# Kernel optimization log

Hardware: AMD Instinct MI355X
Metric: run time of the kernel (lower is better)

## Reference

```python
import jax, jax.numpy as jnp
import numpy as np

N_NODES = 50000
N_EDGES = 800000
DIMS = [100, 512, 256, 128, 200]  # input -> conv1 -> conv2 -> conv3 -> conv4


def setup_inputs() -> dict:
    key = jax.random.key(0)
    ks = jax.random.split(key, 2 + 4)
    x = jax.random.normal(ks[0], (N_NODES, DIMS[0]), dtype=jnp.float32)
    edge_index = jax.random.randint(ks[1], (2, N_EDGES), 0, N_NODES, dtype=jnp.int64)
    inp = {"x": x, "edge_index": edge_index}
    for i in range(4):
        fan_in = DIMS[i]
        W = jax.random.normal(ks[2 + i], (DIMS[i], DIMS[i + 1]), dtype=jnp.float32) * (1.0 / np.sqrt(fan_in)).astype(np.float32)
        b = jnp.zeros((DIMS[i + 1],), dtype=jnp.float32)
        inp[f"W{i + 1}"] = W
        inp[f"b{i + 1}"] = b
    return inp


def _gcn_layer(x, row, col, norm, W, b, n):
    # PyG GCNConv: linear transform first, then normalized scatter-add, then bias.
    h = x @ W                           # [N, out]
    msg = h[row] * norm[:, None]        # [E+N, out] gather + edge scale
    agg = jax.ops.segment_sum(msg, col, num_segments=n)  # scatter-add to targets
    return agg + b


def reference(x, edge_index, W1, b1, W2, b2, W3, b3, W4, b4):
    n = x.shape[0]
    loop = jnp.arange(n, dtype=edge_index.dtype)
    row = jnp.concatenate([edge_index[0], loop])  # sources (with self-loops)
    col = jnp.concatenate([edge_index[1], loop])  # targets (with self-loops)
    deg = jax.ops.segment_sum(jnp.ones_like(col, dtype=x.dtype), col, num_segments=n)
    dinv = jnp.where(deg > 0, jax.lax.rsqrt(deg), 0.0)
    norm = dinv[row] * dinv[col]  # symmetric D^{-1/2}(A+I)D^{-1/2} edge weights

    out = jax.nn.relu(_gcn_layer(x, row, col, norm, W1, b1, n))
    out = jax.nn.relu(_gcn_layer(out, row, col, norm, W2, b2, n))
    out = jax.nn.relu(_gcn_layer(out, row, col, norm, W3, b3, n))
    out = jax.nn.relu(_gcn_layer(out, row, col, norm, W4, b4, n))
    return jnp.mean(out, axis=0, keepdims=True)  # [1, 200]
```

## Files before the change

### kernel.cpp

```cpp
#include <hip/hip_runtime.h>
#include <hip/hip_bf16.h>


#define NN 50000
#define NE 800000
#define PRANGE (NN / 8)
#define CAP 96

typedef __attribute__((ext_vector_type(8))) _Float16 f16x8;
typedef __attribute__((ext_vector_type(4))) float floatx4;
typedef __attribute__((ext_vector_type(2))) float floatx2;

union U16x8 {
    uint4 u4;
    f16x8 h;
    _Float16 e[8];
};

__device__ __forceinline__ void dec16(const unsigned char* p, float* f) {
    uint4 v = *(const uint4*)p;
    unsigned w[4] = {v.x, v.y, v.z, v.w};
#pragma unroll
    for (int k = 0; k < 4; k++) {
        floatx2 lo = __builtin_amdgcn_cvt_pk_f32_fp8(w[k], false);
        floatx2 hi = __builtin_amdgcn_cvt_pk_f32_fp8(w[k], true);
        f[k * 4 + 0] = lo[0];
        f[k * 4 + 1] = lo[1];
        f[k * 4 + 2] = hi[0];
        f[k * 4 + 3] = hi[1];
    }
}

__device__ __forceinline__ uint4 enc16(const float* f) {
    uint4 r;
    unsigned w;
    w = __builtin_amdgcn_cvt_pk_fp8_f32(f[0], f[1], 0, false);
    w = __builtin_amdgcn_cvt_pk_fp8_f32(f[2], f[3], (int)w, true);
    r.x = w;
    w = __builtin_amdgcn_cvt_pk_fp8_f32(f[4], f[5], 0, false);
    w = __builtin_amdgcn_cvt_pk_fp8_f32(f[6], f[7], (int)w, true);
    r.y = w;
    w = __builtin_amdgcn_cvt_pk_fp8_f32(f[8], f[9], 0, false);
    w = __builtin_amdgcn_cvt_pk_fp8_f32(f[10], f[11], (int)w, true);
    r.z = w;
    w = __builtin_amdgcn_cvt_pk_fp8_f32(f[12], f[13], 0, false);
    w = __builtin_amdgcn_cvt_pk_fp8_f32(f[14], f[15], (int)w, true);
    r.w = w;
    return r;
}

__device__ __forceinline__ uint4 dec8_f16(uint2 v) {
    floatx2 f0 = __builtin_amdgcn_cvt_pk_f32_fp8(v.x, false);
    floatx2 f1 = __builtin_amdgcn_cvt_pk_f32_fp8(v.x, true);
    floatx2 f2 = __builtin_amdgcn_cvt_pk_f32_fp8(v.y, false);
    floatx2 f3 = __builtin_amdgcn_cvt_pk_f32_fp8(v.y, true);
    U16x8 o;
    o.e[0] = (_Float16)f0[0]; o.e[1] = (_Float16)f0[1];
    o.e[2] = (_Float16)f1[0]; o.e[3] = (_Float16)f1[1];
    o.e[4] = (_Float16)f2[0]; o.e[5] = (_Float16)f2[1];
    o.e[6] = (_Float16)f3[0]; o.e[7] = (_Float16)f3[1];
    return o.u4;
}

__global__ __launch_bounds__(256) void setup_kernel(
    const void* __restrict__ ei, unsigned* __restrict__ fillc,
    float* __restrict__ out, int* __restrict__ r32, int* __restrict__ c32,
    const float* __restrict__ x, unsigned char* __restrict__ xb,
    const float* __restrict__ W1, const float* __restrict__ W2,
    const float* __restrict__ W3, const float* __restrict__ W4,
    _Float16* __restrict__ w1t, _Float16* __restrict__ w2t,
    _Float16* __restrict__ w3t, _Float16* __restrict__ w4t) {
    int bx = blockIdx.x, t = threadIdx.x;
    if (bx < 196) {
        int tid = bx * 256 + t;
        if (tid < NN) fillc[tid] = 0u;
        if (bx == 0 && t < 200) out[t] = 0.f;
        return;
    }
    if (bx < 196 + 3125) {
        int e = (bx - 196) * 256 + t;
        __shared__ int nz;
        if (t == 0) nz = 0;
        __syncthreads();
        unsigned w = ((const unsigned*)ei)[2 * (size_t)e + 1];
        if (w) atomicOr(&nz, 1);
        __syncthreads();
        int r, c;
        if (nz == 0) {
            r = (int)((const long long*)ei)[e];
            c = (int)((const long long*)ei)[NE + e];
        } else {
            r = ((const int*)ei)[e];
            c = ((const int*)ei)[NE + e];
        }
        r32[e] = r;
        c32[e] = c;
        return;
    }
    if (bx < 196 + 3125 + 1563) {
        int tid = (bx - 196 - 3125) * 256 + t;
        int node = tid >> 3, sub = tid & 7;
        if (node >= NN) return;
        int base = sub * 16;
        float f[16];
#pragma unroll
        for (int i = 0; i < 16; i++) {
            int cc = base + i;
            f[i] = (cc < 100) ? x[(size_t)node * 100 + cc] : 0.f;
        }
        *(uint4*)(xb + (size_t)node * 128 + base) = enc16(f);
        return;
    }
    int b = bx - 196 - 3125 - 1563;
    const float* W;
    _Float16* Wt;
    int K, N, Kpad, tid;
    if (b < 256)      { W = W1; Wt = w1t; K = 100; N = 512; Kpad = 128; tid = b * 256 + t; }
    else if (b < 768) { W = W2; Wt = w2t; K = 512; N = 256; Kpad = 512; tid = (b - 256) * 256 + t; }
    else if (b < 896) { W = W3; Wt = w3t; K = 256; N = 128; Kpad = 256; tid = (b - 768) * 256 + t; }
    else              { W = W4; Wt = w4t; K = 128; N = 200; Kpad = 128; tid = (b - 896) * 256 + t; }
    int n = tid / Kpad, k = tid - n * Kpad;
    float v = (k < K && n < N) ? W[(size_t)k * N + n] : 0.f;
    Wt[tid] = (_Float16)v;
}

__global__ __launch_bounds__(256) void fill_kernel(
    const int* __restrict__ r32, const int* __restrict__ c32,
    unsigned* __restrict__ fillc, int* __restrict__ ep) {
    const int part = blockIdx.x & 7;
    const int lo = part * PRANGE, hi = lo + PRANGE;
    const int group = blockIdx.x >> 3;
    for (int e = group * 256 + threadIdx.x; e < NE; e += 128 * 256) {
        int c = c32[e];
        if (c >= lo && c < hi) {
            int idx = (int)atomicAdd(&fillc[c], 1u);
            if (idx < CAP) ep[c * CAP + idx] = r32[e];
        }
    }
}

template <int D, int BR>
__global__ __launch_bounds__(256) void agg_kernel(
    const unsigned char* __restrict__ H, const int* __restrict__ ep,
    const unsigned* __restrict__ fillc, const float* __restrict__ bias,
    unsigned char* __restrict__ O) {
    constexpr int LPN = D / 16;
    int tid = blockIdx.x * 256 + threadIdx.x;
    int node = tid / LPN;
    int sub = tid % LPN;
    if (node >= NN) return;
    int deg = (int)fillc[node];
    if (deg > CAP) deg = CAP;
    const int s = node * CAP;
    const int e = s + deg;
    float dc = rsqrtf((float)(deg + 1));
    float selfw = dc * dc;
    const int base = sub * 16;
    const unsigned char* __restrict__ Hb = H + base;
    float acc[16], t0[16], t1[16];
    dec16(Hb + (size_t)node * D, t0);
#pragma unroll
    for (int i = 0; i < 16; i++) acc[i] = selfw * t0[i];
    int j = s;
    for (; j + 2 <= e; j += 2) {
        int r0 = ep[j];
        int r1 = ep[j + 1];
        float w0 = rsqrtf((float)((int)fillc[r0] + 1)) * dc;
        float w1 = rsqrtf((float)((int)fillc[r1] + 1)) * dc;
        dec16(Hb + (size_t)r0 * D, t0);
        dec16(Hb + (size_t)r1 * D, t1);
#pragma unroll
        for (int i = 0; i < 16; i++) acc[i] = fmaf(w0, t0[i], acc[i]);
#pragma unroll
        for (int i = 0; i < 16; i++) acc[i] = fmaf(w1, t1[i], acc[i]);
    }
    if (j < e) {
        int r0 = ep[j];
        float w0 = rsqrtf((float)((int)fillc[r0] + 1)) * dc;
        dec16(Hb + (size_t)r0 * D, t0);
#pragma unroll
        for (int i = 0; i < 16; i++) acc[i] = fmaf(w0, t0[i], acc[i]);
    }
    if (BR) {
#pragma unroll
        for (int i = 0; i < 16; i++) acc[i] = fmaxf(acc[i] + bias[base + i], 0.f);
    }
    *(uint4*)(O + (size_t)node * D + base) = enc16(acc);
}

template <int EPI>
__global__ __launch_bounds__(256) void gemm_kernel(
    const unsigned char* __restrict__ A, const _Float16* __restrict__ B,
    const float* __restrict__ bias, unsigned char* __restrict__ Cb,
    float* __restrict__ outmean, int M, int K, int N) {
    __shared__ _Float16 Asl[64 * 36];
    __shared__ _Float16 Bsl[128 * 36];
    __shared__ float red[128];
    const int m0 = blockIdx.y * 64;
    const int n0 = blockIdx.x * 128;
    const int t = threadIdx.x;
    const int lane = t & 63, w = t >> 6;
    const int wm = (w >> 1) * 32, wn = (w & 1) * 64;
    const int r16 = lane & 15, quad = lane >> 4;

    const int arow = t >> 2, ac8 = (t & 3) * 8;
    int gma = m0 + arow; if (gma > M - 1) gma = M - 1;
    const unsigned char* Aptr = A + (size_t)gma * K + ac8;
    const int rb0 = t >> 2, kb0 = (t & 3) * 8;
    const int rb1 = (t + 256) >> 2, kb1 = kb0;
    const _Float16* Bptr0 = B + (size_t)(n0 + rb0) * K + kb0;
    const _Float16* Bptr1 = B + (size_t)(n0 + rb1) * K + kb1;

    floatx4 acc[2][4];
    const floatx4 fz = {0.f, 0.f, 0.f, 0.f};
#pragma unroll
    for (int i = 0; i < 2; i++)
#pragma unroll
        for (int j = 0; j < 4; j++) acc[i][j] = fz;

    uint2 apf = *(const uint2*)Aptr;
    uint4 bpf0 = *(const uint4*)Bptr0;
    uint4 bpf1 = *(const uint4*)Bptr1;

    for (int kc = 0; kc < K; kc += 32) {
        __syncthreads();
        *(uint4*)(Asl + arow * 36 + ac8) = dec8_f16(apf);
        *(uint4*)(Bsl + rb0 * 36 + kb0) = bpf0;
        *(uint4*)(Bsl + rb1 * 36 + kb1) = bpf1;
        __syncthreads();
        if (kc + 32 < K) {
            apf = *(const uint2*)(Aptr + kc + 32);
            bpf0 = *(const uint4*)(Bptr0 + kc + 32);
            bpf1 = *(const uint4*)(Bptr1 + kc + 32);
        }
        f16x8 af[2], bf[4];
#pragma unroll
        for (int i = 0; i < 2; i++)
            af[i] = *(const f16x8*)(Asl + (wm + i * 16 + r16) * 36 + quad * 8);
#pragma unroll
        for (int j = 0; j < 4; j++)
            bf[j] = *(const f16x8*)(Bsl + (wn + j * 16 + r16) * 36 + quad * 8);
#pragma unroll
        for (int i = 0; i < 2; i++)
#pragma unroll
            for (int j = 0; j < 4; j++)
                acc[i][j] = __builtin_amdgcn_mfma_f32_16x16x32_f16(af[i], bf[j], acc[i][j], 0, 0, 0);
    }

    if (EPI == 2) {
        if (t < 128) red[t] = 0.f;
        __syncthreads();
#pragma unroll
        for (int j = 0; j < 4; j++) {
            int col = n0 + wn + j * 16 + r16;
            float s = 0.f;
            if (col < N) {
                float bv = bias[col];
#pragma unroll
                for (int i = 0; i < 2; i++) {
                    int mbase = m0 + wm + i * 16 + quad * 4;
#pragma unroll
                    for (int r = 0; r < 4; r++)
                        if (mbase + r < M) s += fmaxf(acc[i][j][r] + bv, 0.f);
                }
            }
            atomicAdd(&red[wn + j * 16 + r16], s);
        }
        __syncthreads();
        if (t < 128) {
            int col = n0 + t;
            if (col < N) atomicAdd(outmean + col, red[t] * (1.0f / (float)NN));
        }
    } else {
#pragma unroll
        for (int i = 0; i < 2; i++) {
            int mbase = m0 + wm + i * 16 + quad * 4;
#pragma unroll
            for (int r = 0; r < 4; r++) {
                int m = mbase + r;
                if (m >= M) continue;
#pragma unroll
                for (int j = 0; j < 4; j++) {
                    int col = n0 + wn + j * 16 + r16;
                    float v = acc[i][j][r];
                    if (EPI == 1) v = fmaxf(v + bias[col], 0.f);
                    unsigned pk = __builtin_amdgcn_cvt_pk_fp8_f32(v, v, 0, false);
                    Cb[(size_t)m * N + col] = (unsigned char)(pk & 0xffu);
                }
            }
        }
    }
}

extern "C" void kernel_launch(void* const* d_in, const int* in_sizes, int n_in,
                              void* d_out, int out_size, void* d_ws, size_t ws_size,
                              hipStream_t stream) {
    const float* x  = (const float*)d_in[0];
    const void*  ei = d_in[1];
    const float* W1 = (const float*)d_in[2];
    const float* b1 = (const float*)d_in[3];
    const float* W2 = (const float*)d_in[4];
    const float* b2 = (const float*)d_in[5];
    const float* W3 = (const float*)d_in[6];
    const float* b3 = (const float*)d_in[7];
    const float* W4 = (const float*)d_in[8];
    const float* b4 = (const float*)d_in[9];
    float* out = (float*)d_out;

    char* ws = (char*)d_ws;
    size_t o = 0;
    auto alloc = [&](size_t bytes) -> void* {
        void* p = ws + o;
        o += (bytes + 255) & ~(size_t)255;
        return p;
    };
    unsigned* fillc = (unsigned*)alloc((size_t)NN * 4);
    int*      r32   = (int*)alloc((size_t)NE * 4);
    int*      c32   = (int*)alloc((size_t)NE * 4);
    int*      ep    = (int*)alloc((size_t)NN * CAP * 4);
    _Float16* w1t = (_Float16*)alloc((size_t)512 * 128 * 2);
    _Float16* w2t = (_Float16*)alloc((size_t)256 * 512 * 2);
    _Float16* w3t = (_Float16*)alloc((size_t)128 * 256 * 2);
    _Float16* w4t = (_Float16*)alloc((size_t)256 * 128 * 2);
    unsigned char* xb  = (unsigned char*)alloc((size_t)NN * 128);
    unsigned char* A1b = (unsigned char*)alloc((size_t)NN * 128);
    unsigned char* H1b = (unsigned char*)alloc((size_t)NN * 512);
    unsigned char* t2b = (unsigned char*)alloc((size_t)NN * 256);
    unsigned char* H2b = (unsigned char*)alloc((size_t)NN * 256);
    unsigned char* t3b = (unsigned char*)alloc((size_t)NN * 128);
    unsigned char* h3b = (unsigned char*)alloc((size_t)NN * 128);
    unsigned char* A4b = (unsigned char*)alloc((size_t)NN * 128);

    const int PB = 1024;

    setup_kernel<<<196 + 3125 + 1563 + 1024, 256, 0, stream>>>(
        ei, fillc, out, r32, c32, x, xb, W1, W2, W3, W4, w1t, w2t, w3t, w4t);
    fill_kernel<<<PB, 256, 0, stream>>>(r32, c32, fillc, ep);

    const int MB64 = (NN + 63) / 64;
    const int AB128 = (NN * 8 + 255) / 256;
    const int AB256 = (NN * 16 + 255) / 256;

    agg_kernel<128, 0><<<AB128, 256, 0, stream>>>(xb, ep, fillc, nullptr, A1b);
    gemm_kernel<1><<<dim3(4, MB64), 256, 0, stream>>>(A1b, w1t, b1, H1b, nullptr, NN, 128, 512);
    gemm_kernel<0><<<dim3(2, MB64), 256, 0, stream>>>(H1b, w2t, nullptr, t2b, nullptr, NN, 512, 256);
    agg_kernel<256, 1><<<AB256, 256, 0, stream>>>(t2b, ep, fillc, b2, H2b);
    gemm_kernel<0><<<dim3(1, MB64), 256, 0, stream>>>(H2b, w3t, nullptr, t3b, nullptr, NN, 256, 128);
    agg_kernel<128, 1><<<AB128, 256, 0, stream>>>(t3b, ep, fillc, b3, h3b);
    agg_kernel<128, 0><<<AB128, 256, 0, stream>>>(h3b, ep, fillc, nullptr, A4b);
    gemm_kernel<2><<<dim3(2, MB64), 256, 0, stream>>>(A4b, w4t, b4, nullptr, out, NN, 128, 200);
}
```

Before: 314.3 us.

## Fuse neighbor aggregation into following GEMM via shared-memory A tile

Adds an aggemm kernel that gathers and normalizes neighbor rows for a 64-node tile straight into shared memory as fp16, then runs MFMA against the weight matrix with B read directly from global memory. Three agg+gemm pairs are replaced with this fused kernel, which removes the fp8 intermediate round-trips A1b, H2b and A4b and several launches. In exchange, each block now computes all N output columns, so the per-tile gather work is no longer split across column blocks. B is no longer staged in LDS, and the fused kernels launch far fewer blocks than before, which may lower occupancy and latency hiding.

New measurement: 348.7 us. 10.9% more time.

```diff
diff --git a/kernel.cpp b/kernel.cpp
--- a/kernel.cpp
+++ b/kernel.cpp
@@ -139,6 +139,173 @@
     }
 }
 
+__device__ __forceinline__ void gather16(
+    const unsigned char* __restrict__ H, const int* __restrict__ ep,
+    const unsigned* __restrict__ fillc, int node, int K, int base, float* acc) {
+    int deg = (int)fillc[node];
+    if (deg > CAP) deg = CAP;
+    const int s = node * CAP;
+    const int e = s + deg;
+    float dc = rsqrtf((float)(deg + 1));
+    float selfw = dc * dc;
+    const unsigned char* Hb = H + base;
+    float t0[16], t1[16];
+    dec16(Hb + (size_t)node * K, t0);
+#pragma unroll
+    for (int i = 0; i < 16; i++) acc[i] = selfw * t0[i];
+    int j = s;
+    for (; j + 2 <= e; j += 2) {
+        int r0 = ep[j];
+        int r1 = ep[j + 1];
+        float w0 = rsqrtf((float)((int)fillc[r0] + 1)) * dc;
+        float w1 = rsqrtf((float)((int)fillc[r1] + 1)) * dc;
+        dec16(Hb + (size_t)r0 * K, t0);
+        dec16(Hb + (size_t)r1 * K, t1);
+#pragma unroll
+        for (int i = 0; i < 16; i++) acc[i] = fmaf(w0, t0[i], acc[i]);
+#pragma unroll
+        for (int i = 0; i < 16; i++) acc[i] = fmaf(w1, t1[i], acc[i]);
+    }
+    if (j < e) {
+        int r0 = ep[j];
+        float w0 = rsqrtf((float)((int)fillc[r0] + 1)) * dc;
+        dec16(Hb + (size_t)r0 * K, t0);
+#pragma unroll
+        for (int i = 0; i < 16; i++) acc[i] = fmaf(w0, t0[i], acc[i]);
+    }
+}
+
+template <int K, int N, int BR, int EPI>
+__global__ __launch_bounds__(256) void aggemm_kernel(
+    const unsigned char* __restrict__ H, const int* __restrict__ ep,
+    const unsigned* __restrict__ fillc, const float* __restrict__ abias,
+    const _Float16* __restrict__ B, const float* __restrict__ gbias,
+    unsigned char* __restrict__ Cb, float* __restrict__ outmean) {
+    constexpr int NCH = K / 32;
+    __shared__ _Float16 Asl[NCH][64 * 36];
+    __shared__ float red[(EPI == 2) ? N : 1];
+    const int m0 = blockIdx.x * 64;
+    const int t = threadIdx.x;
+
+    constexpr int LPN = K / 16;
+    constexpr int NPP = 256 / LPN;
+#pragma unroll
+    for (int pass = 0; pass < 64 / NPP; pass++) {
+        int row = pass * NPP + t / LPN;
+        int sub = t % LPN;
+        int node = m0 + row;
+        int base = sub * 16;
+        float acc[16];
+        if (node < NN) {
+            gather16(H, ep, fillc, node, K, base, acc);
+            if (BR) {
+#pragma unroll
+                for (int i = 0; i < 16; i++) acc[i] = fmaxf(acc[i] + abias[base + i], 0.f);
+            }
+        } else {
+#pragma unroll
+            for (int i = 0; i < 16; i++) acc[i] = 0.f;
+        }
+        U16x8 o0, o1;
+#pragma unroll
+        for (int i = 0; i < 8; i++) o0.e[i] = (_Float16)acc[i];
+#pragma unroll
+        for (int i = 0; i < 8; i++) o1.e[i] = (_Float16)acc[8 + i];
+        _Float16* dst = &Asl[sub >> 1][row * 36 + (sub & 1) * 16];
+        *(uint4*)dst = o0.u4;
+        *(uint4*)(dst + 8) = o1.u4;
+    }
+    __syncthreads();
+    if (EPI == 2) {
+        for (int i = t; i < N; i += 256) red[i] = 0.f;
+        __syncthreads();
+    }
+
+    const int lane = t & 63, w = t >> 6;
+    const int mh = (w >> 1) * 32;
+    const int nbase = (w & 1) * (N / 2);
+    const int r16 = lane & 15, quad = lane >> 4;
+    constexpr int NSUB = N / 128;
+
+#pragma unroll
+    for (int sc = 0; sc < NSUB; sc++) {
+        const int n0s = nbase + sc * 64;
+        floatx4 acc2[2][4];
+        const floatx4 fz = {0.f, 0.f, 0.f, 0.f};
+#pragma unroll
+        for (int i = 0; i < 2; i++)
+#pragma unroll
+            for (int j = 0; j < 4; j++) acc2[i][j] = fz;
+
+        f16x8 bfp[4];
+#pragma unroll
+        for (int j = 0; j < 4; j++)
+            bfp[j] = *(const f16x8*)(B + (size_t)(n0s + j * 16 + r16) * K + quad * 8);
+
+#pragma unroll
+        for (int kc = 0; kc < K; kc += 32) {
+            f16x8 bf[4];
+#pragma unroll
+            for (int j = 0; j < 4; j++) bf[j] = bfp[j];
+            if (kc + 32 < K) {
+#pragma unroll
+                for (int j = 0; j < 4; j++)
+                    bfp[j] = *(const f16x8*)(B + (size_t)(n0s + j * 16 + r16) * K + kc + 32 + quad * 8);
+            }
+            f16x8 af[2];
+#pragma unroll
+            for (int i = 0; i < 2; i++)
+                af[i] = *(const f16x8*)&Asl[kc / 32][(mh + i * 16 + r16) * 36 + quad * 8];
+#pragma unroll
+            for (int i = 0; i < 2; i++)
+#pragma unroll
+                for (int j = 0; j < 4; j++)
+                    acc2[i][j] = __builtin_amdgcn_mfma_f32_16x16x32_f16(af[i], bf[j], acc2[i][j], 0, 0, 0);
+        }
+
+        if (EPI == 2) {
+#pragma unroll
+            for (int j = 0; j < 4; j++) {
+                int col = n0s + j * 16 + r16;
+                if (col < 200) {
+                    float bv = gbias[col];
+                    float s = 0.f;
+#pragma unroll
+                    for (int i = 0; i < 2; i++) {
+                        int mbase = m0 + mh + i * 16 + quad * 4;
+#pragma unroll
+                        for (int r = 0; r < 4; r++)
+                            if (mbase + r < NN) s += fmaxf(acc2[i][j][r] + bv, 0.f);
+                    }
+                    atomicAdd(&red[col], s);
+                }
+            }
+        } else {
+#pragma unroll
+            for (int i = 0; i < 2; i++) {
+                int mbase = m0 + mh + i * 16 + quad * 4;
+#pragma unroll
+                for (int r = 0; r < 4; r++) {
+                    int m = mbase + r;
+                    if (m >= NN) continue;
+#pragma unroll
+                    for (int j = 0; j < 4; j++) {
+                        int col = n0s + j * 16 + r16;
+                        float v = acc2[i][j][r];
+                        if (EPI == 1) v = fmaxf(v + gbias[col], 0.f);
+                        unsigned pk = __builtin_amdgcn_cvt_pk_fp8_f32(v, v, 0, false);
+                        Cb[(size_t)m * N + col] = (unsigned char)(pk & 0xffu);
+                    }
+                }
+            }
+        }
+    }
+    if (EPI == 2) {
+        __syncthreads();
+        for (int i = t; i < 200; i += 256) atomicAdd(outmean + i, red[i] * (1.0f / (float)NN));
+    }
+}
+
 template <int D, int BR>
 __global__ __launch_bounds__(256) void agg_kernel(
     const unsigned char* __restrict__ H, const int* __restrict__ ep,
@@ -149,38 +316,9 @@
     int node = tid / LPN;
     int sub = tid % LPN;
     if (node >= NN) return;
-    int deg = (int)fillc[node];
-    if (deg > CAP) deg = CAP;
-    const int s = node * CAP;
-    const int e = s + deg;
-    float dc = rsqrtf((float)(deg + 1));
-    float selfw = dc * dc;
-    const int base = sub * 16;
-    const unsigned char* __restrict__ Hb = H + base;
-    float acc[16], t0[16], t1[16];
-    dec16(Hb + (size_t)node * D, t0);
-#pragma unroll
-    for (int i = 0; i < 16; i++) acc[i] = selfw * t0[i];
-    int j = s;
-    for (; j + 2 <= e; j += 2) {
-        int r0 = ep[j];
-        int r1 = ep[j + 1];
-        float w0 = rsqrtf((float)((int)fillc[r0] + 1)) * dc;
-        float w1 = rsqrtf((float)((int)fillc[r1] + 1)) * dc;
-        dec16(Hb + (size_t)r0 * D, t0);
-        dec16(Hb + (size_t)r1 * D, t1);
-#pragma unroll
-        for (int i = 0; i < 16; i++) acc[i] = fmaf(w0, t0[i], acc[i]);
-#pragma unroll
-        for (int i = 0; i < 16; i++) acc[i] = fmaf(w1, t1[i], acc[i]);
-    }
-    if (j < e) {
-        int r0 = ep[j];
-        float w0 = rsqrtf((float)((int)fillc[r0] + 1)) * dc;
-        dec16(Hb + (size_t)r0 * D, t0);
-#pragma unroll
-        for (int i = 0; i < 16; i++) acc[i] = fmaf(w0, t0[i], acc[i]);
-    }
+    int base = sub * 16;
+    float acc[16];
+    gather16(H, ep, fillc, node, D, base, acc);
     if (BR) {
 #pragma unroll
         for (int i = 0; i < 16; i++) acc[i] = fmaxf(acc[i] + bias[base + i], 0.f);
@@ -188,14 +326,11 @@
     *(uint4*)(O + (size_t)node * D + base) = enc16(acc);
 }
 
-template <int EPI>
 __global__ __launch_bounds__(256) void gemm_kernel(
     const unsigned char* __restrict__ A, const _Float16* __restrict__ B,
-    const float* __restrict__ bias, unsigned char* __restrict__ Cb,
-    float* __restrict__ outmean, int M, int K, int N) {
+    unsigned char* __restrict__ Cb, int M, int K, int N) {
     __shared__ _Float16 Asl[64 * 36];
     __shared__ _Float16 Bsl[128 * 36];
-    __shared__ float red[128];
     const int m0 = blockIdx.y * 64;
     const int n0 = blockIdx.x * 128;
     const int t = threadIdx.x;
@@ -247,46 +382,19 @@
                 acc[i][j] = __builtin_amdgcn_mfma_f32_16x16x32_f16(af[i], bf[j], acc[i][j], 0, 0, 0);
     }
 
-    if (EPI == 2) {
-        if (t < 128) red[t] = 0.f;
-        __syncthreads();
-#pragma unroll
-        for (int j = 0; j < 4; j++) {
-            int col = n0 + wn + j * 16 + r16;
-            float s = 0.f;
-            if (col < N) {
-                float bv = bias[col];
-#pragma unroll
-                for (int i = 0; i < 2; i++) {
-                    int mbase = m0 + wm + i * 16 + quad * 4;
-#pragma unroll
-                    for (int r = 0; r < 4; r++)
-                        if (mbase + r < M) s += fmaxf(acc[i][j][r] + bv, 0.f);
-                }
-            }
-            atomicAdd(&red[wn + j * 16 + r16], s);
-        }
-        __syncthreads();
-        if (t < 128) {
-            int col = n0 + t;
-            if (col < N) atomicAdd(outmean + col, red[t] * (1.0f / (float)NN));
-        }
-    } else {
-#pragma unroll
-        for (int i = 0; i < 2; i++) {
-            int mbase = m0 + wm + i * 16 + quad * 4;
-#pragma unroll
-            for (int r = 0; r < 4; r++) {
-                int m = mbase + r;
-                if (m >= M) continue;
-#pragma unroll
-                for (int j = 0; j < 4; j++) {
-                    int col = n0 + wn + j * 16 + r16;
-                    float v = acc[i][j][r];
-                    if (EPI == 1) v = fmaxf(v + bias[col], 0.f);
-                    unsigned pk = __builtin_amdgcn_cvt_pk_fp8_f32(v, v, 0, false);
-                    Cb[(size_t)m * N + col] = (unsigned char)(pk & 0xffu);
-                }
+#pragma unroll
+    for (int i = 0; i < 2; i++) {
+        int mbase = m0 + wm + i * 16 + quad * 4;
+#pragma unroll
+        for (int r = 0; r < 4; r++) {
+            int m = mbase + r;
+            if (m >= M) continue;
+#pragma unroll
+            for (int j = 0; j < 4; j++) {
+                int col = n0 + wn + j * 16 + r16;
+                float v = acc[i][j][r];
+                unsigned pk = __builtin_amdgcn_cvt_pk_fp8_f32(v, v, 0, false);
+                Cb[(size_t)m * N + col] = (unsigned char)(pk & 0xffu);
             }
         }
     }
@@ -323,30 +431,24 @@
     _Float16* w3t = (_Float16*)alloc((size_t)128 * 256 * 2);
     _Float16* w4t = (_Float16*)alloc((size_t)256 * 128 * 2);
     unsigned char* xb  = (unsigned char*)alloc((size_t)NN * 128);
-    unsigned char* A1b = (unsigned char*)alloc((size_t)NN * 128);
     unsigned char* H1b = (unsigned char*)alloc((size_t)NN * 512);
     unsigned char* t2b = (unsigned char*)alloc((size_t)NN * 256);
-    unsigned char* H2b = (unsigned char*)alloc((size_t)NN * 256);
     unsigned char* t3b = (unsigned char*)alloc((size_t)NN * 128);
     unsigned char* h3b = (unsigned char*)alloc((size_t)NN * 128);
-    unsigned char* A4b = (unsigned char*)alloc((size_t)NN * 128);
-
-    const int PB = 1024;
 
     setup_kernel<<<196 + 3125 + 1563 + 1024, 256, 0, stream>>>(
         ei, fillc, out, r32, c32, x, xb, W1, W2, W3, W4, w1t, w2t, w3t, w4t);
-    fill_kernel<<<PB, 256, 0, stream>>>(r32, c32, fillc, ep);
+    fill_kernel<<<1024, 256, 0, stream>>>(r32, c32, fillc, ep);
 
     const int MB64 = (NN + 63) / 64;
     const int AB128 = (NN * 8 + 255) / 256;
-    const int AB256 = (NN * 16 + 255) / 256;
-
-    agg_kernel<128, 0><<<AB128, 256, 0, stream>>>(xb, ep, fillc, nullptr, A1b);
-    gemm_kernel<1><<<dim3(4, MB64), 256, 0, stream>>>(A1b, w1t, b1, H1b, nullptr, NN, 128, 512);
-    gemm_kernel<0><<<dim3(2, MB64), 256, 0, stream>>>(H1b, w2t, nullptr, t2b, nullptr, NN, 512, 256);
-    agg_kernel<256, 1><<<AB256, 256, 0, stream>>>(t2b, ep, fillc, b2, H2b);
-    gemm_kernel<0><<<dim3(1, MB64), 256, 0, stream>>>(H2b, w3t, nullptr, t3b, nullptr, NN, 256, 128);
+
+    aggemm_kernel<128, 512, 0, 1><<<MB64, 256, 0, stream>>>(
+        xb, ep, fillc, nullptr, w1t, b1, H1b, nullptr);
+    gemm_kernel<<<dim3(2, MB64), 256, 0, stream>>>(H1b, w2t, t2b, NN, 512, 256);
+    aggemm_kernel<256, 128, 1, 0><<<MB64, 256, 0, stream>>>(
+        t2b, ep, fillc, b2, w3t, nullptr, t3b, nullptr);
     agg_kernel<128, 1><<<AB128, 256, 0, stream>>>(t3b, ep, fillc, b3, h3b);
-    agg_kernel<128, 0><<<AB128, 256, 0, stream>>>(h3b, ep, fillc, nullptr, A4b);
-    gemm_kernel<2><<<dim3(2, MB64), 256, 0, stream>>>(A4b, w4t, b4, nullptr, out, NN, 128, 200);
-}
+    aggemm_kernel<128, 256, 0, 2><<<MB64, 256, 0, stream>>>(
+        h3b, ep, fillc, nullptr, w4t, b4, nullptr, out);
+}
```
